# Kernel tuning notes

Hardware: AMD Instinct MI355X
Metric: run time of the kernel (lower is better)

## Reference

```python
import jax, jax.numpy as jnp
import numpy as np

DIM = 2048
HEADS = 16
KV_HEADS = 4
DIM_HEAD = 128
INNER = HEADS * DIM_HEAD          # 2048
KV_INNER = KV_HEADS * DIM_HEAD    # 512
FF = 4 * DIM                      # 8192
QK_SCALE = 10.0                   # x-transformers default qk_norm_scale
B, S = 2, 2048


def layer_norm(x, g, b, eps=1e-5):
    m = jnp.mean(x, axis=-1, keepdims=True)
    v = jnp.mean((x - m) ** 2, axis=-1, keepdims=True)
    return (x - m) * jax.lax.rsqrt(v + eps) * g + b


def l2norm(t, eps=1e-12):
    n = jnp.sqrt(jnp.sum(t * t, axis=-1, keepdims=True))
    return t / jnp.maximum(n, eps)


def setup_inputs() -> dict:
    key = jax.random.key(0)
    ks = jax.random.split(key, 12)
    s = lambda fan_in: 1.0 / np.sqrt(fan_in)
    return {
        "x":     jax.random.normal(ks[0], (B, S, DIM), jnp.float32),
        "wq":    jax.random.normal(ks[1], (DIM, INNER), jnp.float32) * s(DIM),
        "wk":    jax.random.normal(ks[2], (DIM, KV_INNER), jnp.float32) * s(DIM),
        "wv":    jax.random.normal(ks[3], (DIM, KV_INNER), jnp.float32) * s(DIM),
        "wo":    jax.random.normal(ks[4], (INNER, DIM), jnp.float32) * s(INNER),
        "ln1_g": jnp.ones((DIM,), jnp.float32),
        "ln1_b": jnp.zeros((DIM,), jnp.float32),
        "w1":    jax.random.normal(ks[5], (DIM, FF), jnp.float32) * s(DIM),
        "b1":    jnp.zeros((FF,), jnp.float32),
        "lnf_g": jnp.ones((FF,), jnp.float32),
        "lnf_b": jnp.zeros((FF,), jnp.float32),
        "w2":    jax.random.normal(ks[6], (FF, DIM), jnp.float32) * s(FF),
        "b2":    jnp.zeros((DIM,), jnp.float32),
    }


def reference(x, wq, wk, wv, wo, ln1_g, ln1_b, w1, b1, lnf_g, lnf_b, w2, b2):
    b, s, _ = x.shape
    rep = HEADS // KV_HEADS
    # GQA projections
    q = (x @ wq).reshape(b, s, HEADS, DIM_HEAD).transpose(0, 2, 1, 3)      # [b,h,s,d]
    k = (x @ wk).reshape(b, s, KV_HEADS, DIM_HEAD).transpose(0, 2, 1, 3)   # [b,g,s,d]
    v = (x @ wv).reshape(b, s, KV_HEADS, DIM_HEAD).transpose(0, 2, 1, 3)
    # qk-norm: l2-normalize q/k along head dim, fixed scale
    q = l2norm(q)
    k = l2norm(k)
    k = jnp.repeat(k, rep, axis=1)  # expand kv heads to query heads
    v = jnp.repeat(v, rep, axis=1)
    scores = jnp.einsum("bhid,bhjd->bhij", q, k) * QK_SCALE
    attn = jax.nn.softmax(scores, axis=-1)
    o = jnp.einsum("bhij,bhjd->bhid", attn, v)
    o = o.transpose(0, 2, 1, 3).reshape(b, s, INNER) @ wo
    # post-attention LayerNorm (no residual in the source)
    h = layer_norm(o, ln1_g, ln1_b)
    # FFN: SiLU + post-activation LayerNorm (dropout inert in eval)
    f = jax.nn.silu(h @ w1 + b1)
    f = layer_norm(f, lnf_g, lnf_b)
    y = f @ w2 + b2
    # the source re-applies the SAME norm after the ffn
    return layer_norm(y, ln1_g, ln1_b)
```

## Files before the change

### kernel.cpp

```cpp
#include <hip/hip_runtime.h>


typedef __attribute__((ext_vector_type(8))) short short8;
typedef __attribute__((ext_vector_type(4))) float f32x4;
typedef __attribute__((ext_vector_type(16))) float f32x16;

__device__ __forceinline__ unsigned short f2bf(float f) {
  unsigned int u = __builtin_bit_cast(unsigned int, f);
  u += 0x7FFFu + ((u >> 16) & 1u);
  return (unsigned short)(u >> 16);
}
__device__ __forceinline__ float bf2f(unsigned short h) {
  unsigned int u = ((unsigned int)h) << 16;
  return __builtin_bit_cast(float, u);
}

typedef const void __attribute__((address_space(1)))* gas1_t;
typedef void __attribute__((address_space(3)))* las3_t;
#define GLDS16(g, l) \
  __builtin_amdgcn_global_load_lds((gas1_t)(const void*)(g), (las3_t)(void*)(l), 16, 0, 0)

__global__ __launch_bounds__(256) void cast_f32_bf16(const float* __restrict__ src,
                                                     unsigned short* __restrict__ dst,
                                                     int n) {
  int i = (blockIdx.x * 256 + threadIdx.x) * 4;
  if (i >= n) return;
  float4 f = *(const float4*)(src + i);
  uint2 u;
  u.x = (unsigned)f2bf(f.x) | ((unsigned)f2bf(f.y) << 16);
  u.y = (unsigned)f2bf(f.z) | ((unsigned)f2bf(f.w) << 16);
  *(uint2*)(dst + i) = u;
}

__global__ __launch_bounds__(256) void transcast64(const float* __restrict__ src,
                                                   unsigned short* __restrict__ dst,
                                                   int R, int C, int dst_ld, int row_off) {
  __shared__ float t[64][65];
  const int tid = threadIdx.x;
  const int tx = tid & 15, ty = tid >> 4;
  const int c0 = blockIdx.x * 64, r0 = blockIdx.y * 64;
#pragma unroll
  for (int j = 0; j < 4; ++j) {
    float4 v = *(const float4*)(src + (size_t)(r0 + j * 16 + ty) * C + c0 + tx * 4);
    t[j * 16 + ty][tx * 4 + 0] = v.x;
    t[j * 16 + ty][tx * 4 + 1] = v.y;
    t[j * 16 + ty][tx * 4 + 2] = v.z;
    t[j * 16 + ty][tx * 4 + 3] = v.w;
  }
  __syncthreads();
  const int cc = tid >> 2, seg = tid & 3;
  unsigned up[8];
#pragma unroll
  for (int i = 0; i < 8; ++i)
    up[i] = (unsigned)f2bf(t[seg * 16 + 2 * i][cc]) |
            ((unsigned)f2bf(t[seg * 16 + 2 * i + 1][cc]) << 16);
  unsigned short* d = dst + (size_t)(row_off + c0 + cc) * dst_ld + r0 + seg * 16;
  *(uint4*)(d) = *(uint4*)&up[0];
  *(uint4*)(d + 8) = *(uint4*)&up[4];
}

template <int KS>
__global__ __launch_bounds__(512, 1) void gemm8ph(const unsigned short* __restrict__ A,
                                                  const unsigned short* __restrict__ Bt,
                                                  unsigned short* __restrict__ C0,
                                                  unsigned short* __restrict__ C1,
                                                  int ldc, int Keff) {
  extern __shared__ char lds[];
  const int tid = threadIdx.x, l = tid & 63, w = tid >> 6;
  const int wr = w >> 2, wc = w & 3;
  const int gx = gridDim.x, gy = gridDim.y;
  const int did = blockIdx.y * gx + blockIdx.x;
  const int q = (gx * gy) >> 3;
  const int tcm = (did & 7) * q + (did >> 3);
  const int brow = (tcm % gy) * 256, bcol = (tcm / gy) * 256;
  const int ld = Keff * KS;
  const unsigned short* Aa = A + (size_t)brow * ld + blockIdx.z * Keff;
  const unsigned short* Bb = Bt + (size_t)bcol * ld + blockIdx.z * Keff;
  unsigned short* C = (KS == 1 || blockIdx.z == 0) ? C0 : C1;
  const int NT = Keff >> 6;

  const int slot = l >> 4;
  const int rowA = wr * 128 + (l & 15);
  const int aRd = ((((rowA << 2) | slot) << 4) ^ ((rowA & 7) << 4));
  const int rowB = wc * 64 + (l & 15);
  const int bRd = ((((rowB << 2) | slot) << 4) ^ ((rowB & 7) << 4));

  f32x4 acc[8][4];
#pragma unroll
  for (int m = 0; m < 8; ++m)
#pragma unroll
    for (int n = 0; n < 4; ++n) acc[m][n] = (f32x4){0.f, 0.f, 0.f, 0.f};

  auto stage = [&](int s) {
    const int tile = s >> 2, kind = s & 3;
    const int kofs = ((tile < NT) ? tile * 64 : 0) + (kind >> 1) * 32;
    const unsigned short* src = (kind & 1) ? Bb : Aa;
    char* dst = lds + (tile & 1) * 65536 + kind * 16384;
#pragma unroll
    for (int r = 0; r < 2; ++r) {
      const int g = r * 512 + tid;
      const int rw = ((g >> 3) << 1) | (((g >> 2) ^ (g >> 4)) & 1);
      const int sl = (g ^ rw) & 3;
      GLDS16(src + (size_t)rw * ld + kofs + sl * 8, dst + g * 16);
    }
  };

#define BAR() __builtin_amdgcn_s_barrier()
#define LGKM0() asm volatile("s_waitcnt lgkmcnt(0)" ::: "memory")
#define VM6() asm volatile("s_waitcnt vmcnt(6)" ::: "memory")
#define MFMA16(AF, BF, MO)                                                     \
  do {                                                                         \
    __builtin_amdgcn_s_setprio(1);                                             \
    _Pragma("unroll") for (int m_ = 0; m_ < 4; ++m_)                           \
        _Pragma("unroll") for (int n_ = 0; n_ < 4; ++n_)                       \
            acc[(MO) + m_][n_] = __builtin_amdgcn_mfma_f32_16x16x32_bf16(      \
                (AF)[m_], (BF)[n_], acc[(MO) + m_][n_], 0, 0, 0);              \
    __builtin_amdgcn_s_setprio(0);                                             \
  } while (0)

  short8 af0[4], af1[4], af2[4], af3[4], bf0[4], bf1[4];

  stage(0); stage(1); stage(2); stage(3); stage(4); stage(5);
  asm volatile("s_waitcnt vmcnt(8)" ::: "memory");
  BAR();
#pragma unroll
  for (int n = 0; n < 4; ++n) bf0[n] = *(const short8*)(lds + 16384 + bRd + n * 1024);
#pragma unroll
  for (int m = 0; m < 4; ++m) af0[m] = *(const short8*)(lds + aRd + m * 1024);

  for (int T = 0; T < NT; ++T) {
    char* cur = lds + (T & 1) * 65536;
    char* nxt = lds + ((T + 1) & 1) * 65536;
    char* A0 = cur, *A1 = cur + 32768, *B1 = cur + 49152;

    stage(4 * T + 6);
    LGKM0();
    BAR();
#pragma unroll
    for (int m = 0; m < 4; ++m) af1[m] = *(const short8*)(A0 + aRd + (4 + m) * 1024);
    MFMA16(af0, bf0, 0);

    stage(4 * T + 7);
    VM6();
    LGKM0();
    BAR();
#pragma unroll
    for (int n = 0; n < 4; ++n) bf1[n] = *(const short8*)(B1 + bRd + n * 1024);
#pragma unroll
    for (int m = 0; m < 4; ++m) af2[m] = *(const short8*)(A1 + aRd + m * 1024);
    MFMA16(af1, bf0, 4);

    stage(4 * T + 8);
    LGKM0();
    BAR();
#pragma unroll
    for (int m = 0; m < 4; ++m) af3[m] = *(const short8*)(A1 + aRd + (4 + m) * 1024);
    MFMA16(af2, bf1, 0);

    stage(4 * T + 9);
    VM6();
    LGKM0();
    BAR();
#pragma unroll
    for (int n = 0; n < 4; ++n) bf0[n] = *(const short8*)(nxt + 16384 + bRd + n * 1024);
#pragma unroll
    for (int m = 0; m < 4; ++m) af0[m] = *(const short8*)(nxt + aRd + m * 1024);
    MFMA16(af3, bf1, 4);
  }
#undef BAR
#undef LGKM0
#undef VM6
#undef MFMA16

#pragma unroll
  for (int m = 0; m < 8; ++m)
#pragma unroll
    for (int r = 0; r < 4; ++r) {
      const int row = brow + wr * 128 + m * 16 + (l >> 4) * 4 + r;
#pragma unroll
      for (int n = 0; n < 4; ++n) {
        const int col = bcol + wc * 64 + n * 16 + (l & 15);
        C[(size_t)row * ldc + col] = f2bf(acc[m][n][r]);
      }
    }
}

__global__ __launch_bounds__(256) void l2norm_qk(unsigned short* __restrict__ qkv) {
  const int wid = blockIdx.x * 4 + (threadIdx.x >> 6);
  const int l = threadIdx.x & 63;
  const int token = wid / 20, u = wid % 20;
  const int col = (u < 16) ? u * 128 : 2048 + (u - 16) * 128;
  unsigned short* p = qkv + (size_t)token * 3072 + col + l * 2;
  const float a = bf2f(p[0]), b = bf2f(p[1]);
  float ss = a * a + b * b;
#pragma unroll
  for (int m = 1; m < 64; m <<= 1) ss += __shfl_xor(ss, m);
  const float sc = ((u < 16) ? 14.4269504089f : 1.f) / fmaxf(sqrtf(ss), 1e-12f);
  p[0] = f2bf(a * sc);
  p[1] = f2bf(b * sc);
}

__global__ __launch_bounds__(256) void vtrans(const unsigned short* __restrict__ qkv,
                                              unsigned short* __restrict__ vt) {
  const int idx = blockIdx.x * 256 + threadIdx.x;
  const int s_ = idx & 2047;
  const int rest = idx >> 11;
  const int d = rest & 127;
  const int bg = rest >> 7;
  const int b = bg >> 2, g = bg & 3;
  vt[idx] = qkv[(size_t)(b * 2048 + s_) * 3072 + 2560 + g * 128 + d];
}

__global__ __launch_bounds__(512) void attn_kernel(const unsigned short* __restrict__ qkv,
                                                   const unsigned short* __restrict__ vt,
                                                   unsigned short* __restrict__ out) {
  extern __shared__ char smem[];
  const int tid = threadIdx.x, w = tid >> 6, l = tid & 63;
  const int hi = l >> 5, l31 = l & 31;

  const int n = blockIdx.x;
  const int np = (n & 7) * 32 + (n >> 3);
  const int qi = np & 7, bh = np >> 3;
  const int b = bh >> 4, h = bh & 15, g = h >> 2;
  const int q0 = qi * 256;

  const unsigned short* kbase = qkv + (size_t)(b * 2048) * 3072 + 2048 + g * 128;
  const unsigned short* vbase = vt + (size_t)(b * 4 + g) * 128 * 2048;

  short8 qf[8];
  {
    const unsigned short* qrow = qkv + (size_t)(b * 2048 + q0 + w * 32 + l31) * 3072 + h * 128;
#pragma unroll
    for (int st = 0; st < 8; ++st)
      qf[st] = *(const short8*)&qrow[st * 16 + hi * 8];
  }

  f32x16 o[4];
#pragma unroll
  for (int d0 = 0; d0 < 4; ++d0)
#pragma unroll
    for (int i = 0; i < 16; ++i) o[d0][i] = 0.f;
  float l_part = 0.f;

  const int krow = tid >> 3, kc = (tid & 7) * 2;
  const int vd = tid >> 2, vc = (tid & 3) * 2;
  const unsigned short* kg = kbase + (size_t)krow * 3072 + kc * 8;
  const unsigned short* vg = vbase + (size_t)vd * 2048 + vc * 8;
  const int ko0 = krow * 256 + ((kc ^ (krow & 15)) << 4);
  const int ko1 = krow * 256 + (((kc + 1) ^ (krow & 15)) << 4);
  const int vrp = vd >> 1, vcl = (vd & 1) * 8;
  const int vo0 = vrp * 256 + (((vcl + vc) ^ (vrp & 15)) << 4);
  const int vo1 = vrp * 256 + (((vcl + vc + 1) ^ (vrp & 15)) << 4);

  {
    uint4 k0 = *(const uint4*)kg, k1 = *(const uint4*)(kg + 8);
    uint4 v0 = *(const uint4*)vg, v1 = *(const uint4*)(vg + 8);
    char* Kb = smem;
    char* Vb = smem + 16384;
    *(uint4*)(Kb + ko0) = k0; *(uint4*)(Kb + ko1) = k1;
    *(uint4*)(Vb + vo0) = v0; *(uint4*)(Vb + vo1) = v1;
  }
  __syncthreads();

  const int swzk = l31 & 15;
  for (int t = 0; t < 32; ++t) {
    uint4 k0, k1, v0, v1;
    const bool more = (t + 1) < 32;
    if (more) {
      const size_t kvo = (size_t)(t + 1) * 64;
      k0 = *(const uint4*)(kg + kvo * 3072);
      k1 = *(const uint4*)(kg + kvo * 3072 + 8);
      v0 = *(const uint4*)(vg + kvo);
      v1 = *(const uint4*)(vg + kvo + 8);
    }

    char* Kb = smem + (t & 1) * 32768;
    char* Vb = Kb + 16384;

    f32x16 s0, s1;
#pragma unroll
    for (int i = 0; i < 16; ++i) { s0[i] = 0.f; s1[i] = 0.f; }
    __builtin_amdgcn_s_setprio(1);
#pragma unroll
    for (int st = 0; st < 8; ++st) {
      const int ch = st * 2 + hi;
      short8 kf0 = *(const short8*)(Kb + l31 * 256 + ((ch ^ swzk) << 4));
      short8 kf1 = *(const short8*)(Kb + (l31 + 32) * 256 + ((ch ^ swzk) << 4));
      s0 = __builtin_amdgcn_mfma_f32_32x32x16_bf16(kf0, qf[st], s0, 0, 0, 0);
      s1 = __builtin_amdgcn_mfma_f32_32x32x16_bf16(kf1, qf[st], s1, 0, 0, 0);
    }
    __builtin_amdgcn_s_setprio(0);

#pragma unroll
    for (int i = 0; i < 16; ++i) {
      s0[i] = exp2f(s0[i]);
      s1[i] = exp2f(s1[i]);
      l_part += s0[i] + s1[i];
    }

    short8 pa[4];
#pragma unroll
    for (int ks = 0; ks < 4; ++ks) {
      const f32x16& sv = (ks < 2) ? s0 : s1;
      const int base = (ks & 1) * 8;
      auto pk = [](float x, float y) -> unsigned {
        unsigned ux = __builtin_bit_cast(unsigned, x);
        unsigned uy = __builtin_bit_cast(unsigned, y);
        return ((uy + 0x8000u) & 0xFFFF0000u) | ((ux + 0x8000u) >> 16);
      };
      unsigned a = pk(sv[base + 0], sv[base + 1]);
      unsigned bq = pk(sv[base + 4], sv[base + 5]);
      unsigned c = pk(sv[base + 2], sv[base + 3]);
      unsigned d = pk(sv[base + 6], sv[base + 7]);
      unsigned as = __shfl_xor(a, 32), bs = __shfl_xor(bq, 32);
      unsigned cs = __shfl_xor(c, 32), ds = __shfl_xor(d, 32);
      uint4 wv;
      wv.x = (l < 32) ? a : bs;
      wv.y = (l < 32) ? c : ds;
      wv.z = (l < 32) ? as : bq;
      wv.w = (l < 32) ? cs : d;
      pa[ks] = __builtin_bit_cast(short8, wv);
    }

    __builtin_amdgcn_s_setprio(1);
#pragma unroll
    for (int ks = 0; ks < 4; ++ks) {
#pragma unroll
      for (int d0 = 0; d0 < 4; ++d0) {
        const int dd = d0 * 32 + l31;
        const int rp = dd >> 1;
        const int cl = ((dd & 1) * 8 + ks * 2 + hi) ^ (rp & 15);
        short8 vf = *(const short8*)(Vb + rp * 256 + (cl << 4));
        o[d0] = __builtin_amdgcn_mfma_f32_32x32x16_bf16(pa[ks], vf, o[d0], 0, 0, 0);
      }
    }
    __builtin_amdgcn_s_setprio(0);

    __syncthreads();
    if (more) {
      char* Kn = smem + ((t + 1) & 1) * 32768;
      char* Vn = Kn + 16384;
      *(uint4*)(Kn + ko0) = k0; *(uint4*)(Kn + ko1) = k1;
      *(uint4*)(Vn + vo0) = v0; *(uint4*)(Vn + vo1) = v1;
    }
    __syncthreads();
  }

  float ltot = l_part + __shfl_xor(l_part, 32);
  float linv = 1.f / ltot;
  const int tok_base = b * 2048 + q0 + w * 32;
#pragma unroll
  for (int r = 0; r < 16; ++r) {
    const int qr = (r & 3) + 8 * (r >> 2) + 4 * hi;
    const float li = __shfl(linv, qr);
    unsigned short* orow = out + (size_t)(tok_base + qr) * 2048 + h * 128 + l31;
#pragma unroll
    for (int d0 = 0; d0 < 4; ++d0)
      orow[d0 * 32] = f2bf(o[d0][r] * li);
  }
}

template <int NC, bool BIAS, bool SILU, bool OUTF32, bool SUM2>
__global__ __launch_bounds__(256) void ln_row(const unsigned short* __restrict__ src,
                                              const unsigned short* __restrict__ src2,
                                              unsigned short* __restrict__ dstb,
                                              float* __restrict__ dstf,
                                              const float* __restrict__ gamma,
                                              const float* __restrict__ beta,
                                              const float* __restrict__ bias) {
  constexpr int E = NC / 256;
  const int row = blockIdx.x, tid = threadIdx.x;
  const size_t base = (size_t)row * NC + tid * E;
  float v[E];
#pragma unroll
  for (int c = 0; c < E / 8; ++c) {
    uint4 u = *(const uint4*)(src + base + c * 8);
    const unsigned short* us = (const unsigned short*)&u;
#pragma unroll
    for (int j = 0; j < 8; ++j) v[c * 8 + j] = bf2f(us[j]);
  }
  if constexpr (SUM2) {
#pragma unroll
    for (int c = 0; c < E / 8; ++c) {
      uint4 u = *(const uint4*)(src2 + base + c * 8);
      const unsigned short* us = (const unsigned short*)&u;
#pragma unroll
      for (int j = 0; j < 8; ++j) v[c * 8 + j] += bf2f(us[j]);
    }
  }
  if constexpr (BIAS) {
#pragma unroll
    for (int i = 0; i < E; ++i) v[i] += bias[tid * E + i];
  }
  if constexpr (SILU) {
#pragma unroll
    for (int i = 0; i < E; ++i) v[i] = v[i] / (1.f + __expf(-v[i]));
  }
  float s = 0.f, q = 0.f;
#pragma unroll
  for (int i = 0; i < E; ++i) {
    s += v[i];
    q += v[i] * v[i];
  }
#pragma unroll
  for (int m = 1; m < 64; m <<= 1) {
    s += __shfl_xor(s, m);
    q += __shfl_xor(q, m);
  }
  __shared__ float rs[4], rq[4];
  if ((tid & 63) == 0) {
    rs[tid >> 6] = s;
    rq[tid >> 6] = q;
  }
  __syncthreads();
  s = rs[0] + rs[1] + rs[2] + rs[3];
  q = rq[0] + rq[1] + rq[2] + rq[3];
  const float mean = s / NC;
  const float rstd = rsqrtf(q / NC - mean * mean + 1e-5f);
#pragma unroll
  for (int i = 0; i < E; ++i)
    v[i] = (v[i] - mean) * rstd * gamma[tid * E + i] + beta[tid * E + i];
  if constexpr (OUTF32) {
#pragma unroll
    for (int c = 0; c < E / 4; ++c) {
      float4 f = {v[c * 4], v[c * 4 + 1], v[c * 4 + 2], v[c * 4 + 3]};
      *(float4*)(dstf + base + c * 4) = f;
    }
  } else {
#pragma unroll
    for (int c = 0; c < E / 8; ++c) {
      uint4 u;
      unsigned* up = (unsigned*)&u;
#pragma unroll
      for (int j = 0; j < 4; ++j)
        up[j] = (unsigned)f2bf(v[c * 8 + j * 2]) | ((unsigned)f2bf(v[c * 8 + j * 2 + 1]) << 16);
      *(uint4*)(dstb + base + c * 8) = u;
    }
  }
}

extern "C" void kernel_launch(void* const* d_in, const int* in_sizes, int n_in,
                              void* d_out, int out_size, void* d_ws, size_t ws_size,
                              hipStream_t stream) {
  (void)in_sizes; (void)n_in; (void)out_size; (void)ws_size;
  const float* x     = (const float*)d_in[0];
  const float* wq    = (const float*)d_in[1];
  const float* wk    = (const float*)d_in[2];
  const float* wv    = (const float*)d_in[3];
  const float* wo    = (const float*)d_in[4];
  const float* ln1_g = (const float*)d_in[5];
  const float* ln1_b = (const float*)d_in[6];
  const float* w1    = (const float*)d_in[7];
  const float* b1    = (const float*)d_in[8];
  const float* lnf_g = (const float*)d_in[9];
  const float* lnf_b = (const float*)d_in[10];
  const float* w2    = (const float*)d_in[11];
  const float* b2    = (const float*)d_in[12];

  unsigned short* ws = (unsigned short*)d_ws;
  unsigned short* wqkvT  = ws;
  unsigned short* woT    = wqkvT  + (size_t)3072 * 2048;
  unsigned short* w1T    = woT    + (size_t)2048 * 2048;
  unsigned short* w2T    = w1T    + (size_t)8192 * 2048;
  unsigned short* xb     = w2T    + (size_t)2048 * 8192;
  unsigned short* qkv    = xb     + (size_t)4096 * 2048;
  unsigned short* vt     = qkv    + (size_t)4096 * 3072;
  unsigned short* attn_o = vt     + (size_t)4096 * 512;
  unsigned short* f1     = attn_o + (size_t)4096 * 2048;

  (void)hipFuncSetAttribute((const void*)gemm8ph<1>,
                            hipFuncAttributeMaxDynamicSharedMemorySize, 131072);
  (void)hipFuncSetAttribute((const void*)gemm8ph<2>,
                            hipFuncAttributeMaxDynamicSharedMemorySize, 131072);
  (void)hipFuncSetAttribute((const void*)attn_kernel,
                            hipFuncAttributeMaxDynamicSharedMemorySize, 65536);

  cast_f32_bf16<<<8192, 256, 0, stream>>>(x, xb, 4096 * 2048);
  transcast64<<<dim3(32, 32),  256, 0, stream>>>(wq, wqkvT, 2048, 2048, 2048, 0);
  transcast64<<<dim3(8, 32),   256, 0, stream>>>(wk, wqkvT, 2048, 512, 2048, 2048);
  transcast64<<<dim3(8, 32),   256, 0, stream>>>(wv, wqkvT, 2048, 512, 2048, 2560);
  transcast64<<<dim3(32, 32),  256, 0, stream>>>(wo, woT, 2048, 2048, 2048, 0);
  transcast64<<<dim3(128, 32), 256, 0, stream>>>(w1, w1T, 2048, 8192, 2048, 0);
  transcast64<<<dim3(32, 128), 256, 0, stream>>>(w2, w2T, 8192, 2048, 8192, 0);

  gemm8ph<1><<<dim3(12, 16, 1), 512, 131072, stream>>>(xb, wqkvT, qkv, nullptr, 3072, 2048);
  l2norm_qk<<<20480, 256, 0, stream>>>(qkv);
  vtrans<<<8192, 256, 0, stream>>>(qkv, vt);
  attn_kernel<<<256, 512, 65536, stream>>>(qkv, vt, attn_o);
  gemm8ph<2><<<dim3(8, 16, 2), 512, 131072, stream>>>(attn_o, woT, qkv, f1, 2048, 1024);
  ln_row<2048, false, false, false, true><<<4096, 256, 0, stream>>>(
      qkv, f1, xb, nullptr, ln1_g, ln1_b, nullptr);
  gemm8ph<1><<<dim3(32, 16, 1), 512, 131072, stream>>>(xb, w1T, f1, nullptr, 8192, 2048);
  ln_row<8192, true, true, false, false><<<4096, 256, 0, stream>>>(
      f1, nullptr, f1, nullptr, lnf_g, lnf_b, b1);
  gemm8ph<2><<<dim3(8, 16, 2), 512, 131072, stream>>>(f1, w2T, xb, attn_o, 2048, 4096);
  ln_row<2048, true, false, true, true><<<4096, 256, 0, stream>>>(
      xb, attn_o, nullptr, (float*)d_out, ln1_g, ln1_b, b2);
}
```

Before: 654.4 us.

## Drop fragment register prefetch in GEMM main loop and widen cast kernel

```diff
diff --git a/kernel.cpp b/kernel.cpp
--- a/kernel.cpp
+++ b/kernel.cpp
@@ -23,13 +23,16 @@
 __global__ __launch_bounds__(256) void cast_f32_bf16(const float* __restrict__ src,
                                                      unsigned short* __restrict__ dst,
                                                      int n) {
-  int i = (blockIdx.x * 256 + threadIdx.x) * 4;
+  int i = (blockIdx.x * 256 + threadIdx.x) * 8;
   if (i >= n) return;
-  float4 f = *(const float4*)(src + i);
-  uint2 u;
-  u.x = (unsigned)f2bf(f.x) | ((unsigned)f2bf(f.y) << 16);
-  u.y = (unsigned)f2bf(f.z) | ((unsigned)f2bf(f.w) << 16);
-  *(uint2*)(dst + i) = u;
+  float4 a = *(const float4*)(src + i);
+  float4 b = *(const float4*)(src + i + 4);
+  uint4 u;
+  u.x = (unsigned)f2bf(a.x) | ((unsigned)f2bf(a.y) << 16);
+  u.y = (unsigned)f2bf(a.z) | ((unsigned)f2bf(a.w) << 16);
+  u.z = (unsigned)f2bf(b.x) | ((unsigned)f2bf(b.y) << 16);
+  u.w = (unsigned)f2bf(b.z) | ((unsigned)f2bf(b.w) << 16);
+  *(uint4*)(dst + i) = u;
 }
 
 __global__ __launch_bounds__(256) void transcast64(const float* __restrict__ src,
@@ -105,8 +108,9 @@
     }
   };
 
-#define BAR() __builtin_amdgcn_s_barrier()
-#define LGKM0() asm volatile("s_waitcnt lgkmcnt(0)" ::: "memory")
+#define BAR() asm volatile("s_barrier" ::: "memory")
+#define LGKM0() do { asm volatile("s_waitcnt lgkmcnt(0)" ::: "memory"); \
+                     __builtin_amdgcn_sched_barrier(0); } while (0)
 #define VM6() asm volatile("s_waitcnt vmcnt(6)" ::: "memory")
 #define MFMA16(AF, BF, MO)                                                     \
   do {                                                                         \
@@ -118,54 +122,49 @@
     __builtin_amdgcn_s_setprio(0);                                             \
   } while (0)
 
-  short8 af0[4], af1[4], af2[4], af3[4], bf0[4], bf1[4];
+  short8 af[4], bf[4];
 
   stage(0); stage(1); stage(2); stage(3); stage(4); stage(5);
   asm volatile("s_waitcnt vmcnt(8)" ::: "memory");
   BAR();
-#pragma unroll
-  for (int n = 0; n < 4; ++n) bf0[n] = *(const short8*)(lds + 16384 + bRd + n * 1024);
-#pragma unroll
-  for (int m = 0; m < 4; ++m) af0[m] = *(const short8*)(lds + aRd + m * 1024);
 
   for (int T = 0; T < NT; ++T) {
     char* cur = lds + (T & 1) * 65536;
-    char* nxt = lds + ((T + 1) & 1) * 65536;
-    char* A0 = cur, *A1 = cur + 32768, *B1 = cur + 49152;
-
+    char* A0 = cur, *B0 = cur + 16384, *A1 = cur + 32768, *B1 = cur + 49152;
+
+#pragma unroll
+    for (int n = 0; n < 4; ++n) bf[n] = *(const short8*)(B0 + bRd + n * 1024);
+#pragma unroll
+    for (int m = 0; m < 4; ++m) af[m] = *(const short8*)(A0 + aRd + m * 1024);
     stage(4 * T + 6);
+    BAR();
     LGKM0();
+    MFMA16(af, bf, 0);
+
+    VM6();
+#pragma unroll
+    for (int m = 0; m < 4; ++m) af[m] = *(const short8*)(A0 + aRd + (4 + m) * 1024);
+    stage(4 * T + 7);
     BAR();
-#pragma unroll
-    for (int m = 0; m < 4; ++m) af1[m] = *(const short8*)(A0 + aRd + (4 + m) * 1024);
-    MFMA16(af0, bf0, 0);
-
-    stage(4 * T + 7);
+    LGKM0();
+    MFMA16(af, bf, 4);
+
+#pragma unroll
+    for (int n = 0; n < 4; ++n) bf[n] = *(const short8*)(B1 + bRd + n * 1024);
+#pragma unroll
+    for (int m = 0; m < 4; ++m) af[m] = *(const short8*)(A1 + aRd + m * 1024);
+    stage(4 * T + 8);
+    BAR();
+    LGKM0();
+    MFMA16(af, bf, 0);
+
     VM6();
+#pragma unroll
+    for (int m = 0; m < 4; ++m) af[m] = *(const short8*)(A1 + aRd + (4 + m) * 1024);
+    stage(4 * T + 9);
+    BAR();
     LGKM0();
-    BAR();
-#pragma unroll
-    for (int n = 0; n < 4; ++n) bf1[n] = *(const short8*)(B1 + bRd + n * 1024);
-#pragma unroll
-    for (int m = 0; m < 4; ++m) af2[m] = *(const short8*)(A1 + aRd + m * 1024);
-    MFMA16(af1, bf0, 4);
-
-    stage(4 * T + 8);
-    LGKM0();
-    BAR();
-#pragma unroll
-    for (int m = 0; m < 4; ++m) af3[m] = *(const short8*)(A1 + aRd + (4 + m) * 1024);
-    MFMA16(af2, bf1, 0);
-
-    stage(4 * T + 9);
-    VM6();
-    LGKM0();
-    BAR();
-#pragma unroll
-    for (int n = 0; n < 4; ++n) bf0[n] = *(const short8*)(nxt + 16384 + bRd + n * 1024);
-#pragma unroll
-    for (int m = 0; m < 4; ++m) af0[m] = *(const short8*)(nxt + aRd + m * 1024);
-    MFMA16(af3, bf1, 4);
+    MFMA16(af, bf, 4);
   }
 #undef BAR
 #undef LGKM0
@@ -475,7 +474,7 @@
   (void)hipFuncSetAttribute((const void*)attn_kernel,
                             hipFuncAttributeMaxDynamicSharedMemorySize, 65536);
 
-  cast_f32_bf16<<<8192, 256, 0, stream>>>(x, xb, 4096 * 2048);
+  cast_f32_bf16<<<4096, 256, 0, stream>>>(x, xb, 4096 * 2048);
   transcast64<<<dim3(32, 32),  256, 0, stream>>>(wq, wqkvT, 2048, 2048, 2048, 0);
   transcast64<<<dim3(8, 32),   256, 0, stream>>>(wk, wqkvT, 2048, 512, 2048, 2048);
   transcast64<<<dim3(8, 32),   256, 0, stream>>>(wv, wqkvT, 2048, 512, 2048, 2560);
```

Measured after the change: 647.3 us. No clear change (-1.1%).
